# Optimization experiments

Measured on AMD Instinct MI355X. Metric: run time of the kernel, lower is better.

## Reference

```python
import jax, jax.numpy as jnp
import numpy as np
from jax import lax

PATCH = 32  # enc conv kernel/stride
EPS = 1e-12  # F.normalize eps


def setup_inputs() -> dict:
    key = jax.random.key(0)
    ks = jax.random.split(key, 7)
    B, N, H, W = 32, 256, 32, 32
    fdim, vdim = 512, 128
    x = jax.random.normal(ks[0], (B, 3 * N, H, W), dtype=jnp.float32)
    conv_w = jax.random.normal(ks[1], (fdim, 3, PATCH, PATCH), dtype=jnp.float32) * (1.0 / np.sqrt(3 * PATCH * PATCH))
    conv_b = jax.random.normal(ks[2], (fdim,), dtype=jnp.float32) * 0.01
    fc1_w = jax.random.normal(ks[3], (vdim, fdim), dtype=jnp.float32) * (1.0 / np.sqrt(fdim))
    fc1_b = jax.random.normal(ks[4], (vdim,), dtype=jnp.float32) * 0.01
    # deterministic dropout masks (p=0.5, train mode -> keep * 1/(1-p))
    drop1 = (jax.random.uniform(ks[5], (B, N, N)) >= 0.5).astype(jnp.float32) * 2.0
    drop2 = (jax.random.uniform(ks[6], (B, N, N)) >= 0.5).astype(jnp.float32) * 2.0
    return {"x": x, "conv_w": conv_w, "conv_b": conv_b,
            "fc1_w": fc1_w, "fc1_b": fc1_b, "drop1": drop1, "drop2": drop2}


def _branch(scores, drop, eye):
    # softmax over dim=-2, zero diag, dropout, L1-normalize over dim=-2
    P = jax.nn.softmax(scores, axis=-2)
    P = P * (1.0 - eye)
    P = P * drop
    denom = jnp.maximum(jnp.sum(jnp.abs(P), axis=-2, keepdims=True), EPS)
    return P / denom


def reference(x, conv_w, conv_b, fc1_w, fc1_b, drop1, drop2):
    B, C, H, W = x.shape
    N = C // 3
    xi = x.reshape(B * N, 3, H, W)
    # enc: patchify conv -> (B*N, fdim, 1, 1)
    fm = lax.conv_general_dilated(xi, conv_w, (PATCH, PATCH), 'VALID',
                                  dimension_numbers=('NCHW', 'OIHW', 'NCHW'))
    fm = fm + conv_b[None, :, None, None]
    # map2vec: adaptive avgpool(1,1) + flatten + fc1
    v = fm.mean(axis=(2, 3))                      # (B*N, fdim)
    v = v @ fc1_w.T + fc1_b                       # (B*N, vdim)
    f = v.reshape(B, N, -1)                       # (B, N, vdim)
    f_norm = f / jnp.maximum(jnp.linalg.norm(f, axis=-1, keepdims=True), EPS)
    A = jnp.einsum('bnd,bmd->bnm', f_norm, f_norm)  # cosine affinity (B,N,N)
    Atemp = A * (128.0 ** 0.5)                    # torch.div(A, 1/128**0.5)
    eye = jnp.eye(N, dtype=A.dtype)
    A1 = _branch(Atemp, drop1, eye)
    A2t = _branch(jnp.swapaxes(Atemp, -1, -2), drop2, eye)
    AtA = jnp.swapaxes(jnp.matmul(A2t, A1), -1, -2)
    # nll_loss(AtA, arange targets) == -mean of diagonal entries
    diag = jnp.einsum('bii->bi', AtA)
    loss = -jnp.mean(diag)
    return f, A, loss
```

## Files before the change

### kernel.cpp

```cpp
#include <hip/hip_runtime.h>
#include <stdint.h>

#define S_SCALE 11.313708498984761f
#define EPS 1e-12f

typedef __bf16 bf16x8 __attribute__((ext_vector_type(8)));
typedef float  f32x4  __attribute__((ext_vector_type(4)));

__device__ __forceinline__ f32x4 mfma16(bf16x8 a, bf16x8 b, f32x4 c) {
  return __builtin_amdgcn_mfma_f32_16x16x32_bf16(a, b, c, 0, 0, 0);
}

__device__ __forceinline__ float waveSum(float v) {
#pragma unroll
  for (int m = 32; m > 0; m >>= 1) v += __shfl_xor(v, m, 64);
  return v;
}

__device__ __forceinline__ void load_lds16(const float* g, float* l) {
  __builtin_amdgcn_global_load_lds(
      (const __attribute__((address_space(1))) uint32_t*)g,
      (__attribute__((address_space(3))) uint32_t*)l, 16, 0, 0);
}

#define OFF_W    0
#define OFF_BIAS 786432
#define OFF_FN   786944
#define OFF_ZP   2884096
#define OFF_P1   3146240

__global__ __launch_bounds__(256) void k_bias(const float* __restrict__ fc1_w,
                                              const float* __restrict__ conv_b,
                                              const float* __restrict__ fc1_b,
                                              float* __restrict__ bias2,
                                              float* __restrict__ loss) {
  const int o = blockIdx.x, t = threadIdx.x;
  if (o == 0 && t == 0) loss[0] = 0.f;
  float p = fc1_w[o * 512 + t] * conv_b[t] +
            fc1_w[o * 512 + 256 + t] * conv_b[256 + t];
  p = waveSum(p);
  __shared__ float red[4];
  if ((t & 63) == 0) red[t >> 6] = p;
  __syncthreads();
  if (t == 0) bias2[o] = red[0] + red[1] + red[2] + red[3] + fc1_b[o];
}

__global__ __launch_bounds__(256) void k_fusew2(const float* __restrict__ conv_w,
                                                const float* __restrict__ fc1_w,
                                                __bf16* __restrict__ W) {
  __shared__ float cw_s[64][36];
  __shared__ float fc1_s[128][65];
  const int t = threadIdx.x;
  const int kt = blockIdx.x;
  const int k0 = kt * 32;
  const int og = t >> 3, kg = t & 7;
  float acc[4][4] = {};
  for (int cs = 0; cs < 8; ++cs) {
    const int cc = cs * 64;
    __syncthreads();
#pragma unroll
    for (int i = 0; i < 8; ++i) {
      int idx = t + 256 * i;
      int cr = idx >> 5, kk = idx & 31;
      cw_s[cr][kk] = conv_w[(cc + cr) * 3072 + k0 + kk];
    }
#pragma unroll
    for (int i = 0; i < 8; ++i) {
      int idx = t + 256 * i;
      int o = idx >> 4, c4 = (idx & 15) * 4;
      float4 v = *(const float4*)&fc1_w[o * 512 + cc + c4];
      fc1_s[o][c4 + 0] = v.x; fc1_s[o][c4 + 1] = v.y;
      fc1_s[o][c4 + 2] = v.z; fc1_s[o][c4 + 3] = v.w;
    }
    __syncthreads();
    for (int ci = 0; ci < 64; ++ci) {
      float4 cw = *(const float4*)&cw_s[ci][kg * 4];
#pragma unroll
      for (int j = 0; j < 4; ++j) {
        float fv = fc1_s[og * 4 + j][ci];
        acc[j][0] = fmaf(fv, cw.x, acc[j][0]);
        acc[j][1] = fmaf(fv, cw.y, acc[j][1]);
        acc[j][2] = fmaf(fv, cw.z, acc[j][2]);
        acc[j][3] = fmaf(fv, cw.w, acc[j][3]);
      }
    }
  }
#pragma unroll
  for (int j = 0; j < 4; ++j)
#pragma unroll
    for (int q = 0; q < 4; ++q)
      W[(og * 4 + j) * 3072 + k0 + kg * 4 + q] = (__bf16)acc[j][q];
}

__global__ __launch_bounds__(256) void k_gemm1(const float* __restrict__ x,
                                               const __bf16* __restrict__ W,
                                               float* __restrict__ P0,
                                               float* __restrict__ P1) {
  __shared__ __align__(16) float A_lds[32 * 64];
  const int t = threadIdx.x;
  const int wave = t >> 6, lane = t & 63;
  const int l15 = lane & 15, quad = lane >> 4;
  const int m0 = blockIdx.x * 32;
  const int kbase = blockIdx.y * 1536;
  float* P = blockIdx.y ? P1 : P0;

  int dr[2], dc[2];
#pragma unroll
  for (int j = 0; j < 2; ++j) {
    int row = wave * 8 + j * 4 + (lane >> 4);
    int cl = (lane & 15) ^ (row & 15);
    dr[j] = row;
    dc[j] = cl * 4;
  }

  f32x4 acc[2][2] = {{{0.f,0.f,0.f,0.f},{0.f,0.f,0.f,0.f}},
                     {{0.f,0.f,0.f,0.f},{0.f,0.f,0.f,0.f}}};
  const __bf16* bp = W + (wave * 32 + l15) * 3072 + quad * 8;

  for (int it = 0; it < 24; ++it) {
    const int k0 = kbase + it * 64;
    __syncthreads();
#pragma unroll
    for (int j = 0; j < 2; ++j)
      load_lds16(x + (m0 + dr[j]) * 3072 + k0 + dc[j],
                 &A_lds[(wave * 2 + j) * 256]);
    uint4 breg[2][2];
#pragma unroll
    for (int ks = 0; ks < 2; ++ks)
#pragma unroll
      for (int ni = 0; ni < 2; ++ni)
        breg[ks][ni] = *(const uint4*)(bp + ni * 16 * 3072 + k0 + ks * 32);
    __syncthreads();
#pragma unroll
    for (int ks = 0; ks < 2; ++ks) {
      bf16x8 afrag[2];
#pragma unroll
      for (int mi = 0; mi < 2; ++mi) {
        const int rb = (l15 + mi * 16) * 64;
        float4 lo = *(const float4*)&A_lds[rb + (((ks * 8 + quad * 2 + 0) ^ l15) << 2)];
        float4 hi = *(const float4*)&A_lds[rb + (((ks * 8 + quad * 2 + 1) ^ l15) << 2)];
        union { __bf16 h[8]; bf16x8 v; } pk;
        pk.h[0] = (__bf16)lo.x; pk.h[1] = (__bf16)lo.y;
        pk.h[2] = (__bf16)lo.z; pk.h[3] = (__bf16)lo.w;
        pk.h[4] = (__bf16)hi.x; pk.h[5] = (__bf16)hi.y;
        pk.h[6] = (__bf16)hi.z; pk.h[7] = (__bf16)hi.w;
        afrag[mi] = pk.v;
      }
#pragma unroll
      for (int mi = 0; mi < 2; ++mi)
#pragma unroll
        for (int ni = 0; ni < 2; ++ni)
          acc[mi][ni] = mfma16(afrag[mi], *(const bf16x8*)&breg[ks][ni],
                               acc[mi][ni]);
    }
  }
#pragma unroll
  for (int mi = 0; mi < 2; ++mi)
#pragma unroll
    for (int ni = 0; ni < 2; ++ni) {
      int col = wave * 32 + ni * 16 + l15;
#pragma unroll
      for (int r = 0; r < 4; ++r) {
        int row = m0 + mi * 16 + quad * 4 + r;
        P[row * 128 + col] = acc[mi][ni][r];
      }
    }
}

__global__ __launch_bounds__(256) void k_fin(float* __restrict__ f_inout,
                                             const float* __restrict__ P1,
                                             const float* __restrict__ bias2,
                                             __bf16* __restrict__ fn) {
  const int wave = threadIdx.x >> 6, lane = threadIdx.x & 63;
  const int row = blockIdx.x * 4 + wave;
  const int i0 = row * 128 + lane, i1 = i0 + 64;
  float v0 = f_inout[i0] + P1[i0] + bias2[lane];
  float v1 = f_inout[i1] + P1[i1] + bias2[lane + 64];
  float ss = waveSum(fmaf(v0, v0, v1 * v1));
  float inv = 1.f / fmaxf(sqrtf(ss), EPS);
  f_inout[i0] = v0;
  f_inout[i1] = v1;
  fn[i0] = (__bf16)(v0 * inv);
  fn[i1] = (__bf16)(v1 * inv);
}

__global__ __launch_bounds__(256) void k_gemm2(const __bf16* __restrict__ fn,
                                               const float* __restrict__ d1,
                                               const float* __restrict__ d2,
                                               float* __restrict__ Aout,
                                               float* __restrict__ Zp) {
  __shared__ __align__(16) __bf16 Li[64][136];
  __shared__ __align__(16) __bf16 Lj[64][136];
  __shared__ float zred[2][4][64];
  const int t = threadIdx.x;
  const int b = blockIdx.y;
  const int ti = blockIdx.x >> 2, tj = blockIdx.x & 3;
  const int i0 = ti * 64, j0 = tj * 64;
  const int wave = t >> 6, lane = t & 63;
  const int l15 = lane & 15, quad = lane >> 4;
  const __bf16* fb = fn + b * 32768;
#pragma unroll
  for (int i = 0; i < 4; ++i) {
    int idx = t + 256 * i;
    int r = idx >> 4, c8 = (idx & 15) * 8;
    *(uint4*)&Li[r][c8] = *(const uint4*)&fb[(i0 + r) * 128 + c8];
    *(uint4*)&Lj[r][c8] = *(const uint4*)&fb[(j0 + r) * 128 + c8];
  }
  __syncthreads();
  f32x4 acc[4] = {{0.f, 0.f, 0.f, 0.f}, {0.f, 0.f, 0.f, 0.f},
                  {0.f, 0.f, 0.f, 0.f}, {0.f, 0.f, 0.f, 0.f}};
#pragma unroll
  for (int ks = 0; ks < 4; ++ks) {
    bf16x8 af = *(const bf16x8*)&Li[wave * 16 + l15][ks * 32 + quad * 8];
#pragma unroll
    for (int nt = 0; nt < 4; ++nt) {
      bf16x8 bf = *(const bf16x8*)&Lj[nt * 16 + l15][ks * 32 + quad * 8];
      acc[nt] = mfma16(af, bf, acc[nt]);
    }
  }
  const int base = b * 65536;
  float* Ab = Aout + base;
  float z1c[4] = {0.f, 0.f, 0.f, 0.f}, z2c[4] = {0.f, 0.f, 0.f, 0.f};
#pragma unroll
  for (int nt = 0; nt < 4; ++nt) {
    int gj = j0 + nt * 16 + l15;
#pragma unroll
    for (int r = 0; r < 4; ++r) {
      int gi = i0 + wave * 16 + quad * 4 + r;
      float a = acc[nt][r];
      Ab[gi * 256 + gj] = a;
      float e = __expf(fmaf(S_SCALE, a, -S_SCALE));
      if (gi != gj) {
        int idx = base + gi * 256 + gj;
        z1c[nt] = fmaf(e, d1[idx], z1c[nt]);
        z2c[nt] = fmaf(e, d2[idx], z2c[nt]);
      }
    }
  }
#pragma unroll
  for (int nt = 0; nt < 4; ++nt) {
    z1c[nt] += __shfl_xor(z1c[nt], 16, 64);
    z1c[nt] += __shfl_xor(z1c[nt], 32, 64);
    z2c[nt] += __shfl_xor(z2c[nt], 16, 64);
    z2c[nt] += __shfl_xor(z2c[nt], 32, 64);
  }
  if (quad == 0) {
#pragma unroll
    for (int nt = 0; nt < 4; ++nt) {
      zred[0][wave][nt * 16 + l15] = z1c[nt];
      zred[1][wave][nt * 16 + l15] = z2c[nt];
    }
  }
  __syncthreads();
  if (t < 128) {
    int z = t >> 6, c = t & 63;
    float s = zred[z][0][c] + zred[z][1][c] + zred[z][2][c] + zred[z][3][c];
    Zp[(z * 4 + ti) * 8192 + b * 256 + j0 + c] = s;
  }
}

__global__ __launch_bounds__(256) void k_loss(const float* __restrict__ Aout,
                                              const float* __restrict__ d1,
                                              const float* __restrict__ d2,
                                              const float* __restrict__ Zp,
                                              float* __restrict__ loss) {
  __shared__ float d1s[64][65];
  __shared__ float z1s[64], z2s[64];
  __shared__ float red[4];
  const int t = threadIdx.x;
  const int b = blockIdx.y;
  const int ic = blockIdx.x >> 2, kc = blockIdx.x & 3;
  const int i0 = ic * 64, k0 = kc * 64;
  const int base = b * 65536;
  if (t < 64) {
    float s = 0.f;
#pragma unroll
    for (int p = 0; p < 4; ++p) s += Zp[p * 8192 + b * 256 + i0 + t];
    z1s[t] = 1.f / fmaxf(s, EPS);
  } else if (t < 128) {
    float s = 0.f;
#pragma unroll
    for (int p = 0; p < 4; ++p) s += Zp[(4 + p) * 8192 + b * 256 + k0 + t - 64];
    z2s[t - 64] = 1.f / fmaxf(s, EPS);
  }
#pragma unroll
  for (int ii = 0; ii < 16; ++ii) {
    int idx = t + 256 * ii;
    int kr = idx >> 6, ci = idx & 63;
    d1s[kr][ci] = d1[base + (k0 + kr) * 256 + i0 + ci];
  }
  __syncthreads();
  const int kl = t & 63, ig = t >> 6;
  float inv2 = z2s[kl];
  float accv = 0.f;
  for (int ii = 0; ii < 16; ++ii) {
    int il = ig * 16 + ii;
    int idx = base + (i0 + il) * 256 + k0 + kl;
    float a = Aout[idx];
    float e = __expf(fmaf(2.f * S_SCALE, a, -2.f * S_SCALE));
    float v = e * d2[idx] * d1s[kl][il] * z1s[il] * inv2;
    if (i0 + il != k0 + kl) accv += v;
  }
  accv = waveSum(accv);
  if ((t & 63) == 0) red[t >> 6] = accv;
  __syncthreads();
  if (t == 0) {
    float tot = red[0] + red[1] + red[2] + red[3];
    atomicAdd(loss, tot * (-1.f / 8192.f));
  }
}

extern "C" void kernel_launch(void* const* d_in, const int* in_sizes, int n_in,
                              void* d_out, int out_size, void* d_ws,
                              size_t ws_size, hipStream_t stream) {
  const float* x = (const float*)d_in[0];
  const float* conv_w = (const float*)d_in[1];
  const float* conv_b = (const float*)d_in[2];
  const float* fc1_w = (const float*)d_in[3];
  const float* fc1_b = (const float*)d_in[4];
  const float* drop1 = (const float*)d_in[5];
  const float* drop2 = (const float*)d_in[6];
  char* ws = (char*)d_ws;
  __bf16* W = (__bf16*)(ws + OFF_W);
  float* bias2 = (float*)(ws + OFF_BIAS);
  __bf16* fn = (__bf16*)(ws + OFF_FN);
  float* Zp = (float*)(ws + OFF_ZP);
  float* P1 = (float*)(ws + OFF_P1);
  float* f = (float*)d_out;
  float* Aout = f + 1048576;
  float* loss = f + 3145728;

  k_bias<<<128, 256, 0, stream>>>(fc1_w, conv_b, fc1_b, bias2, loss);
  k_fusew2<<<96, 256, 0, stream>>>(conv_w, fc1_w, W);
  k_gemm1<<<dim3(256, 2), 256, 0, stream>>>(x, W, f, P1);
  k_fin<<<2048, 256, 0, stream>>>(f, P1, bias2, fn);
  k_gemm2<<<dim3(16, 32), 256, 0, stream>>>(fn, drop1, drop2, Aout, Zp);
  k_loss<<<dim3(16, 32), 256, 0, stream>>>(Aout, drop1, drop2, Zp, loss);
}
```

Measured before the change: 238.5 us.

## Double-buffer gemm1 loads, split K four ways, fold bias kernel into fusew2

The patch GEMM now double-buffers its LDS A tile and B registers, so the next K-step's global loads are issued while the current step's MFMAs run. It also splits K into four partitions instead of two, doubling the grid to 1024 blocks, and sets a min-occupancy launch bound. The bias reduction kernel is merged into an extra block of the weight-fusion kernel, removing one launch. The costs are two extra 4 MB partial buffers that k_fin must read and sum, plus higher register and LDS use per block.

```diff
diff --git a/kernel.cpp b/kernel.cpp
--- a/kernel.cpp
+++ b/kernel.cpp
@@ -29,28 +29,29 @@
 #define OFF_ZP   2884096
 #define OFF_P1   3146240
 
-__global__ __launch_bounds__(256) void k_bias(const float* __restrict__ fc1_w,
-                                              const float* __restrict__ conv_b,
-                                              const float* __restrict__ fc1_b,
-                                              float* __restrict__ bias2,
-                                              float* __restrict__ loss) {
-  const int o = blockIdx.x, t = threadIdx.x;
-  if (o == 0 && t == 0) loss[0] = 0.f;
-  float p = fc1_w[o * 512 + t] * conv_b[t] +
-            fc1_w[o * 512 + 256 + t] * conv_b[256 + t];
-  p = waveSum(p);
-  __shared__ float red[4];
-  if ((t & 63) == 0) red[t >> 6] = p;
-  __syncthreads();
-  if (t == 0) bias2[o] = red[0] + red[1] + red[2] + red[3] + fc1_b[o];
-}
-
 __global__ __launch_bounds__(256) void k_fusew2(const float* __restrict__ conv_w,
                                                 const float* __restrict__ fc1_w,
-                                                __bf16* __restrict__ W) {
+                                                const float* __restrict__ conv_b,
+                                                const float* __restrict__ fc1_b,
+                                                __bf16* __restrict__ W,
+                                                float* __restrict__ bias2,
+                                                float* __restrict__ loss) {
+  const int t = threadIdx.x;
+  const int wave = t >> 6, lane = t & 63;
+  if (blockIdx.x == 96) {
+    if (t == 0) loss[0] = 0.f;
+    for (int o = wave; o < 128; o += 4) {
+      float p = 0.f;
+#pragma unroll
+      for (int c8 = 0; c8 < 8; ++c8)
+        p = fmaf(fc1_w[o * 512 + c8 * 64 + lane], conv_b[c8 * 64 + lane], p);
+      p = waveSum(p);
+      if (lane == 0) bias2[o] = p + fc1_b[o];
+    }
+    return;
+  }
   __shared__ float cw_s[64][36];
   __shared__ float fc1_s[128][65];
-  const int t = threadIdx.x;
   const int kt = blockIdx.x;
   const int k0 = kt * 32;
   const int og = t >> 3, kg = t & 7;
@@ -92,17 +93,60 @@
       W[(og * 4 + j) * 3072 + k0 + kg * 4 + q] = (__bf16)acc[j][q];
 }
 
-__global__ __launch_bounds__(256) void k_gemm1(const float* __restrict__ x,
-                                               const __bf16* __restrict__ W,
-                                               float* __restrict__ P0,
-                                               float* __restrict__ P1) {
-  __shared__ __align__(16) float A_lds[32 * 64];
+
+#define A_READS(BUF, AV)                                                      \
+  _Pragma("unroll") for (int ks = 0; ks < 2; ++ks)                            \
+      _Pragma("unroll") for (int mi = 0; mi < 2; ++mi) {                      \
+    const int rb = (l15 + mi * 16) * 64;                                      \
+    AV[ks][mi][0] =                                                           \
+        *(const float4*)&A_lds[BUF][rb + (((ks * 8 + quad * 2) ^ l15) << 2)]; \
+    AV[ks][mi][1] =                                                           \
+        *(const float4*)&A_lds[BUF][rb + (((ks * 8 + quad * 2 + 1) ^ l15) << 2)]; \
+  }
+
+#define PREFETCH(IT, BUF, BB)                                                 \
+  {                                                                           \
+    const int kn = kbase + (IT) * 64;                                         \
+    _Pragma("unroll") for (int j = 0; j < 2; ++j)                             \
+        load_lds16(x + (m0 + dr[j]) * 3072 + kn + dc[j],                      \
+                   &A_lds[BUF][(wave * 2 + j) * 256]);                        \
+    _Pragma("unroll") for (int ks = 0; ks < 2; ++ks)                          \
+        _Pragma("unroll") for (int ni = 0; ni < 2; ++ni)                      \
+            BB[ks][ni] = *(const uint4*)(bp0 + ni * 49152 + (IT) * 64 + ks * 32); \
+  }
+
+#define COMPUTE(AV, BB)                                                       \
+  _Pragma("unroll") for (int ks = 0; ks < 2; ++ks) {                          \
+    bf16x8 afrag[2];                                                          \
+    _Pragma("unroll") for (int mi = 0; mi < 2; ++mi) {                        \
+      union { __bf16 h[8]; bf16x8 v; } pk;                                    \
+      float4 lo = AV[ks][mi][0], hi = AV[ks][mi][1];                          \
+      pk.h[0] = (__bf16)lo.x; pk.h[1] = (__bf16)lo.y;                         \
+      pk.h[2] = (__bf16)lo.z; pk.h[3] = (__bf16)lo.w;                         \
+      pk.h[4] = (__bf16)hi.x; pk.h[5] = (__bf16)hi.y;                         \
+      pk.h[6] = (__bf16)hi.z; pk.h[7] = (__bf16)hi.w;                         \
+      afrag[mi] = pk.v;                                                       \
+    }                                                                         \
+    _Pragma("unroll") for (int mi = 0; mi < 2; ++mi)                          \
+        _Pragma("unroll") for (int ni = 0; ni < 2; ++ni)                      \
+            acc[mi][ni] =                                                     \
+        mfma16(afrag[mi], *(const bf16x8*)&BB[ks][ni], acc[mi][ni]);          \
+  }
+
+__global__ __launch_bounds__(256, 4) void k_gemm1(const float* __restrict__ x,
+                                                  const __bf16* __restrict__ W,
+                                                  float* __restrict__ P0,
+                                                  float* __restrict__ P1,
+                                                  float* __restrict__ P2,
+                                                  float* __restrict__ P3) {
+  __shared__ __align__(16) float A_lds[2][32 * 64];
   const int t = threadIdx.x;
   const int wave = t >> 6, lane = t & 63;
   const int l15 = lane & 15, quad = lane >> 4;
   const int m0 = blockIdx.x * 32;
-  const int kbase = blockIdx.y * 1536;
-  float* P = blockIdx.y ? P1 : P0;
+  const int kbase = blockIdx.y * 768;
+  float* const Ps[4] = {P0, P1, P2, P3};
+  float* P = Ps[blockIdx.y];
 
   int dr[2], dc[2];
 #pragma unroll
@@ -112,47 +156,24 @@
     dr[j] = row;
     dc[j] = cl * 4;
   }
+  const __bf16* bp0 = W + (wave * 32 + l15) * 3072 + quad * 8 + kbase;
 
   f32x4 acc[2][2] = {{{0.f,0.f,0.f,0.f},{0.f,0.f,0.f,0.f}},
                      {{0.f,0.f,0.f,0.f},{0.f,0.f,0.f,0.f}}};
-  const __bf16* bp = W + (wave * 32 + l15) * 3072 + quad * 8;
-
-  for (int it = 0; it < 24; ++it) {
-    const int k0 = kbase + it * 64;
+  uint4 bA[2][2], bB[2][2];
+  float4 av[2][2][2];
+
+  PREFETCH(0, 0, bA)
+  for (int it2 = 0; it2 < 6; ++it2) {
+    const int it = it2 * 2;
     __syncthreads();
-#pragma unroll
-    for (int j = 0; j < 2; ++j)
-      load_lds16(x + (m0 + dr[j]) * 3072 + k0 + dc[j],
-                 &A_lds[(wave * 2 + j) * 256]);
-    uint4 breg[2][2];
-#pragma unroll
-    for (int ks = 0; ks < 2; ++ks)
-#pragma unroll
-      for (int ni = 0; ni < 2; ++ni)
-        breg[ks][ni] = *(const uint4*)(bp + ni * 16 * 3072 + k0 + ks * 32);
+    A_READS(0, av)
+    if (it + 1 < 12) PREFETCH(it + 1, 1, bB)
+    COMPUTE(av, bA)
     __syncthreads();
-#pragma unroll
-    for (int ks = 0; ks < 2; ++ks) {
-      bf16x8 afrag[2];
-#pragma unroll
-      for (int mi = 0; mi < 2; ++mi) {
-        const int rb = (l15 + mi * 16) * 64;
-        float4 lo = *(const float4*)&A_lds[rb + (((ks * 8 + quad * 2 + 0) ^ l15) << 2)];
-        float4 hi = *(const float4*)&A_lds[rb + (((ks * 8 + quad * 2 + 1) ^ l15) << 2)];
-        union { __bf16 h[8]; bf16x8 v; } pk;
-        pk.h[0] = (__bf16)lo.x; pk.h[1] = (__bf16)lo.y;
-        pk.h[2] = (__bf16)lo.z; pk.h[3] = (__bf16)lo.w;
-        pk.h[4] = (__bf16)hi.x; pk.h[5] = (__bf16)hi.y;
-        pk.h[6] = (__bf16)hi.z; pk.h[7] = (__bf16)hi.w;
-        afrag[mi] = pk.v;
-      }
-#pragma unroll
-      for (int mi = 0; mi < 2; ++mi)
-#pragma unroll
-        for (int ni = 0; ni < 2; ++ni)
-          acc[mi][ni] = mfma16(afrag[mi], *(const bf16x8*)&breg[ks][ni],
-                               acc[mi][ni]);
-    }
+    A_READS(1, av)
+    if (it + 2 < 12) PREFETCH(it + 2, 0, bA)
+    COMPUTE(av, bB)
   }
 #pragma unroll
   for (int mi = 0; mi < 2; ++mi)
@@ -169,13 +190,15 @@
 
 __global__ __launch_bounds__(256) void k_fin(float* __restrict__ f_inout,
                                              const float* __restrict__ P1,
+                                             const float* __restrict__ P2,
+                                             const float* __restrict__ P3,
                                              const float* __restrict__ bias2,
                                              __bf16* __restrict__ fn) {
   const int wave = threadIdx.x >> 6, lane = threadIdx.x & 63;
   const int row = blockIdx.x * 4 + wave;
   const int i0 = row * 128 + lane, i1 = i0 + 64;
-  float v0 = f_inout[i0] + P1[i0] + bias2[lane];
-  float v1 = f_inout[i1] + P1[i1] + bias2[lane + 64];
+  float v0 = f_inout[i0] + P1[i0] + P2[i0] + P3[i0] + bias2[lane];
+  float v1 = f_inout[i1] + P1[i1] + P2[i1] + P3[i1] + bias2[lane + 64];
   float ss = waveSum(fmaf(v0, v0, v1 * v1));
   float inv = 1.f / fmaxf(sqrtf(ss), EPS);
   f_inout[i0] = v0;
@@ -326,14 +349,15 @@
   __bf16* fn = (__bf16*)(ws + OFF_FN);
   float* Zp = (float*)(ws + OFF_ZP);
   float* P1 = (float*)(ws + OFF_P1);
+  float* P2 = P1 + 1048576;
+  float* P3 = P2 + 1048576;
   float* f = (float*)d_out;
   float* Aout = f + 1048576;
   float* loss = f + 3145728;
 
-  k_bias<<<128, 256, 0, stream>>>(fc1_w, conv_b, fc1_b, bias2, loss);
-  k_fusew2<<<96, 256, 0, stream>>>(conv_w, fc1_w, W);
-  k_gemm1<<<dim3(256, 2), 256, 0, stream>>>(x, W, f, P1);
-  k_fin<<<2048, 256, 0, stream>>>(f, P1, bias2, fn);
+  k_fusew2<<<97, 256, 0, stream>>>(conv_w, fc1_w, conv_b, fc1_b, W, bias2, loss);
+  k_gemm1<<<dim3(256, 4), 256, 0, stream>>>(x, W, f, P1, P2, P3);
+  k_fin<<<2048, 256, 0, stream>>>(f, P1, P2, P3, bias2, fn);
   k_gemm2<<<dim3(16, 32), 256, 0, stream>>>(fn, drop1, drop2, Aout, Zp);
   k_loss<<<dim3(16, 32), 256, 0, stream>>>(Aout, drop1, drop2, Zp, loss);
 }
```

Measured after the change: 248.3 us. 1.04x slower.
